# Optimization experiments

Hardware: AMD Instinct MI355X
Metric: run time of the kernel (lower is better)

Reference implementation:

```python
import jax, jax.numpy as jnp
import numpy as np

B, S, IN, H = 32, 512, 512, 1024


def setup_inputs() -> dict:
    key = jax.random.key(0)
    k1, k2, k3 = jax.random.split(key, 3)
    x = jax.random.normal(k1, (B, S, IN), dtype=jnp.float32)
    # Linear weights: [4H, fan_in], init scaled like nn.Linear (~1/sqrt(fan_in))
    W0 = jax.random.normal(k2, (4 * H, IN + H), dtype=jnp.float32) * (1.0 / np.sqrt(IN + H))
    W1 = jax.random.normal(k3, (4 * H, H + H), dtype=jnp.float32) * (1.0 / np.sqrt(H + H))
    b0 = jnp.zeros((4 * H,), dtype=jnp.float32)
    b1 = jnp.zeros((4 * H,), dtype=jnp.float32)
    return {"x": x, "W0": W0, "b0": b0, "W1": W1, "b1": b1}


def _run_layer(inp, W, b):
    """Run one unidirectional LSTM layer over time with lax.scan.

    inp: [B, S, D_in]; W: [4H, D_in+H]; b: [4H].
    Returns (outputs [B, S, H], h_n [B, H], c_n [B, H]).
    """
    h_size = W.shape[0] // 4
    bsz = inp.shape[0]

    def step(carry, x_t):
        h, c = carry
        combined = jnp.concatenate([x_t, h], axis=1)          # [B, D_in+H]
        gates = combined @ W.T + b                            # [B, 4H]
        i, f, g, o = jnp.split(gates, 4, axis=1)
        i = jax.nn.sigmoid(i)
        f = jax.nn.sigmoid(f)
        g = jnp.tanh(g)
        o = jax.nn.sigmoid(o)
        c_next = f * c + i * g
        h_next = o * jnp.tanh(c_next)
        return (h_next, c_next), h_next

    h0 = jnp.zeros((bsz, h_size), dtype=inp.dtype)
    c0 = jnp.zeros((bsz, h_size), dtype=inp.dtype)
    (h_n, c_n), ys = jax.lax.scan(step, (h0, c0), jnp.swapaxes(inp, 0, 1))
    return jnp.swapaxes(ys, 0, 1), h_n, c_n


def reference(x, W0, b0, W1, b1):
    out0, h0n, c0n = _run_layer(x, W0, b0)
    out1, h1n, c1n = _run_layer(out0, W1, b1)
    h_n = jnp.stack([h0n, h1n], axis=0)   # [num_layers, B, H]
    c_n = jnp.stack([c0n, c1n], axis=0)
    return out1[:, -1, :], h_n, c_n
```

## Files before the change

kernel.cpp:

```cpp
#include <hip/hip_runtime.h>


typedef unsigned short ushort_t;
typedef unsigned long long u64_t;
typedef __attribute__((ext_vector_type(8))) short short8;
typedef __attribute__((ext_vector_type(4))) float f32x4;
typedef __attribute__((ext_vector_type(4))) unsigned uint4v;

#define NWG       256
#define NTHREADS  512
#define SEQ       512
#define HSLOT     32768
#define FULLSLOTS 513
#define ABORT_U32 8128
#define CNT_BYTES 32768
#define POLL_MAX  6000

__device__ __forceinline__ ushort_t f2bf(float f) {
  unsigned u = __builtin_bit_cast(unsigned, f);
  u += 0x7FFFu + ((u >> 16) & 1u);
  return (ushort_t)(u >> 16);
}

__device__ __forceinline__ short8 pack_bf8(f32x4 a, f32x4 b) {
  short8 r;
  r[0] = (short)f2bf(a[0]); r[1] = (short)f2bf(a[1]);
  r[2] = (short)f2bf(a[2]); r[3] = (short)f2bf(a[3]);
  r[4] = (short)f2bf(b[0]); r[5] = (short)f2bf(b[1]);
  r[6] = (short)f2bf(b[2]); r[7] = (short)f2bf(b[3]);
  return r;
}

__device__ __forceinline__ float sigm(float x) { return 1.0f / (1.0f + __expf(-x)); }
__device__ __forceinline__ float fast_tanh(float x) {
  x = fminf(fmaxf(x, -15.f), 15.f);
  float e = __expf(-2.0f * x);
  return (1.0f - e) / (1.0f + e);
}

__device__ __forceinline__ unsigned aload(const unsigned* p) {
  return __hip_atomic_load(p, __ATOMIC_RELAXED, __HIP_MEMORY_SCOPE_AGENT);
}

template<bool COH>
__device__ __forceinline__ void load16g(f32x4* hv, const char* base) {
#pragma unroll
  for (int ch = 0; ch < 16; ++ch) {
    const char* a = base + (long)ch * 2048;
    if constexpr (COH)
      asm volatile("global_load_dwordx4 %0, %1, off sc0 sc1"
                   : "=v"(hv[ch]) : "v"(a));
    else
      asm volatile("global_load_dwordx4 %0, %1, off"
                   : "=v"(hv[ch]) : "v"(a));
  }
  asm volatile("s_waitcnt vmcnt(0)" ::: "memory");
  __builtin_amdgcn_sched_barrier(0);
}

__device__ __forceinline__ int bad16(const f32x4* hv) {
  int bad = 0;
#pragma unroll
  for (int ch = 0; ch < 16; ++ch) {
    uint4v d = __builtin_bit_cast(uint4v, hv[ch]);
    unsigned m0 = d[0] > d[1] ? d[0] : d[1];
    unsigned m1 = d[2] > d[3] ? d[2] : d[3];
    unsigned m  = m0 > m1 ? m0 : m1;
    bad |= (int)(m == 0xFFFFFFFFu);
  }
  return bad;
}

template<bool FIRSTCOH>
__device__ __forceinline__ void poll16(f32x4* hv, const char* base,
                                       unsigned* abortp) {
  load16g<FIRSTCOH>(hv, base);
  if (!__any(bad16(hv))) return;
  for (int it = 0;; ++it) {
    load16g<true>(hv, base);
    if (!__any(bad16(hv))) return;
    if ((it & 63) == 63 && aload(abortp) != 0) return;
    if (it >= POLL_MAX) {
      __hip_atomic_store(abortp, 1u, __ATOMIC_RELAXED, __HIP_MEMORY_SCOPE_AGENT);
      return;
    }
    if (it > 8) __builtin_amdgcn_s_sleep(2);
  }
}

template<int KX, bool XFP32, bool ISL1>
__device__ __forceinline__ void run_layer(
    const void* xsrc, long x_step, long x_bstride,
    const ushort_t* __restrict__ hbuf, ushort_t* __restrict__ hbuf_w,
    const float* __restrict__ W, int ldw,
    const float* __restrict__ bias,
    float* __restrict__ out, int out_h_off, int out_c_off, int write_last,
    float* xbuf, float* red, unsigned* abortp, int ub)
{
  constexpr int XCH = (KX / 2) / 32;
  const int lane  = threadIdx.x & 63;
  const int wave  = threadIdx.x >> 6;
  const int ntile = wave >> 2;
  const int r     = wave & 3;
  const bool isH  = r < 2;
  const int sub   = r & 1;
  const int wrow  = lane & 15;
  const int kg    = lane >> 4;
  const int koff  = kg * 8;
  const int bb    = ntile * 16 + (lane & 15);

  const int kbase = isH ? (KX + sub * 512) : ((r - 2) * (KX / 2));
  const int mych  = isH ? 16 : XCH;
  short8 wreg[2][16];
  #pragma unroll
  for (int mt = 0; mt < 2; ++mt) {
    const int grow = (wrow & 3) * 1024 + ub + mt * 4 + (wrow >> 2);
    const float* ws = W + (long)grow * ldw + kbase + koff;
    #pragma unroll
    for (int ch = 0; ch < 16; ++ch) {
      if (ch < mych) {
        f32x4 v0 = *(const f32x4*)(ws + ch * 32);
        f32x4 v1 = *(const f32x4*)(ws + ch * 32 + 4);
        wreg[mt][ch] = pack_bf8(v0, v1);
      }
    }
  }

  const int u0 = ub + kg;
  float bI[2], bF[2], bG[2], bO[2], c[2] = {0.f, 0.f};
  #pragma unroll
  for (int mt = 0; mt < 2; ++mt) {
    const int u = u0 + mt * 4;
    bI[mt] = bias[u];        bF[mt] = bias[1024 + u];
    bG[mt] = bias[2048 + u]; bO[mt] = bias[3072 + u];
  }

  for (int w = 0; w <= SEQ; ++w) {
    const int t = w - 1;
    f32x4 acc[2] = {{0.f,0.f,0.f,0.f},{0.f,0.f,0.f,0.f}};

    if (isH && w >= 1) {
      const char* gb = (const char*)hbuf + (long)t * (HSLOT * 2)
                     + (long)(((sub * 64 + kg) * 32 + bb) * 16);
      f32x4 hv[16];
      poll16<true>(hv, gb, abortp);
      #pragma unroll
      for (int ch = 0; ch < 16; ++ch) {
        short8 b = __builtin_bit_cast(short8, hv[ch]);
        acc[0] = __builtin_amdgcn_mfma_f32_16x16x32_bf16(wreg[0][ch], b, acc[0], 0, 0, 0);
        acc[1] = __builtin_amdgcn_mfma_f32_16x16x32_bf16(wreg[1][ch], b, acc[1], 0, 0, 0);
      }
      if (sub == 0) {
        #pragma unroll
        for (int mt = 0; mt < 2; ++mt)
          *(f32x4*)&red[((ntile * 2 + mt) * 64 + lane) * 4] = acc[mt];
      }
    }

    __syncthreads();

    if (isH && sub == 1 && w >= 1) {
      u64_t pk[2]; float hh[2];
      #pragma unroll
      for (int mt = 0; mt < 2; ++mt) {
        f32x4 a = acc[mt];
        a += *(const f32x4*)&red[((ntile * 2 + mt) * 64 + lane) * 4];
        a += *(const f32x4*)&xbuf[(((((t & 1) * 2 + ntile) * 2 + 0) * 2 + mt) * 64 + lane) * 4];
        a += *(const f32x4*)&xbuf[(((((t & 1) * 2 + ntile) * 2 + 1) * 2 + mt) * 64 + lane) * 4];
        float pi = a[0] + bI[mt], pf = a[1] + bF[mt];
        float pg = a[2] + bG[mt], po = a[3] + bO[mt];
        float ig = sigm(pi), fg = sigm(pf), gg = fast_tanh(pg), og = sigm(po);
        c[mt] = fg * c[mt] + ig * gg;
        float h = og * fast_tanh(c[mt]);
        hh[mt] = h;
        unsigned v  = f2bf(h);
        unsigned v1 = __shfl((int)v, (lane & 15) + 16);
        unsigned v2 = __shfl((int)v, (lane & 15) + 32);
        unsigned v3 = __shfl((int)v, (lane & 15) + 48);
        pk[mt] = (u64_t)(v & 0xFFFFu) | ((u64_t)(v1 & 0xFFFFu) << 16)
               | ((u64_t)(v2 & 0xFFFFu) << 32) | ((u64_t)(v3 & 0xFFFFu) << 48);
      }
      if (t == SEQ - 1) {
        #pragma unroll
        for (int mt = 0; mt < 2; ++mt) {
          const int u = u0 + mt * 4;
          out[out_h_off + bb * 1024 + u] = hh[mt];
          out[out_c_off + bb * 1024 + u] = c[mt];
          if (write_last) out[bb * 1024 + u] = hh[mt];
        }
      }
      if (lane < 16) {
        u64_t* dst = (u64_t*)((char*)hbuf_w + (long)(t + 1) * (HSLOT * 2)
                              + (long)((((ub >> 3) * 32 + bb)) * 16));
        __hip_atomic_store(dst,     pk[0], __ATOMIC_RELAXED, __HIP_MEMORY_SCOPE_AGENT);
        __hip_atomic_store(dst + 1, pk[1], __ATOMIC_RELAXED, __HIP_MEMORY_SCOPE_AGENT);
      }
    }

    if (!isH && w < SEQ) {
      const int s = w;
      f32x4 xa[2] = {{0.f,0.f,0.f,0.f},{0.f,0.f,0.f,0.f}};
      if constexpr (XFP32) {
        const float* bp = (const float*)xsrc + (long)s * x_step
                          + (long)bb * x_bstride + kbase + koff;
        f32x4 xv[2 * XCH];
        #pragma unroll
        for (int ch = 0; ch < XCH; ++ch) {
          xv[2*ch]   = *(const f32x4*)(bp + ch * 32);
          xv[2*ch+1] = *(const f32x4*)(bp + ch * 32 + 4);
        }
        #pragma unroll
        for (int ch = 0; ch < XCH; ++ch) {
          short8 bf = pack_bf8(xv[2*ch], xv[2*ch+1]);
          xa[0] = __builtin_amdgcn_mfma_f32_16x16x32_bf16(wreg[0][ch], bf, xa[0], 0, 0, 0);
          xa[1] = __builtin_amdgcn_mfma_f32_16x16x32_bf16(wreg[1][ch], bf, xa[1], 0, 0, 0);
        }
      } else {
        const char* gb = (const char*)xsrc + (long)s * (HSLOT * 2)
                       + (long)((((r - 2) * 64 + kg) * 32 + bb) * 16);
        f32x4 xv[16];
        poll16<false>(xv, gb, abortp);
        #pragma unroll
        for (int ch = 0; ch < 16; ++ch) {
          short8 b = __builtin_bit_cast(short8, xv[ch]);
          xa[0] = __builtin_amdgcn_mfma_f32_16x16x32_bf16(wreg[0][ch], b, xa[0], 0, 0, 0);
          xa[1] = __builtin_amdgcn_mfma_f32_16x16x32_bf16(wreg[1][ch], b, xa[1], 0, 0, 0);
        }
      }
      #pragma unroll
      for (int mt = 0; mt < 2; ++mt)
        *(f32x4*)&xbuf[(((((s & 1) * 2 + ntile) * 2 + (r - 2)) * 2 + mt) * 64 + lane) * 4] = xa[mt];
    }

    __syncthreads();
  }
}

__global__ __launch_bounds__(NTHREADS, 2)
void lstm_persistent(const float* __restrict__ x,  const float* __restrict__ W0,
                     const float* __restrict__ b0, const float* __restrict__ W1,
                     const float* __restrict__ b1, float* __restrict__ out,
                     unsigned* cnt, ushort_t* O0, ushort_t* H1)
{
  __shared__ float xbuf[4096];
  __shared__ float red[1024];
  const int role = (int)(blockIdx.x >> 7);
  const int ub   = (int)(blockIdx.x & 127) * 8;
  unsigned* abortp = cnt + ABORT_U32;

  if (role == 0) {
    run_layer<512, true, false>(x, 512, 262144,
                                O0, O0, W0, 1536, b0,
                                out, 32768, 98304, 0,
                                xbuf, red, abortp, ub);
  } else {
    run_layer<1024, false, true>((const void*)(O0 + HSLOT), HSLOT, 1024,
                                 H1, H1, W1, 2048, b1,
                                 out, 65536, 131072, 1,
                                 xbuf, red, abortp, ub);
  }
}

extern "C" void kernel_launch(void* const* d_in, const int* in_sizes, int n_in,
                              void* d_out, int out_size, void* d_ws, size_t ws_size,
                              hipStream_t stream) {
  (void)in_sizes; (void)n_in; (void)out_size;

  const float* x  = (const float*)d_in[0];
  const float* W0 = (const float*)d_in[1];
  const float* b0 = (const float*)d_in[2];
  const float* W1 = (const float*)d_in[3];
  const float* b1 = (const float*)d_in[4];
  float* out = (float*)d_out;

  const size_t hb_bytes = (size_t)FULLSLOTS * HSLOT * sizeof(ushort_t);
  const size_t need     = CNT_BYTES + 2 * hb_bytes;
  if (ws_size < need) return;

  unsigned* cnt = (unsigned*)d_ws;
  ushort_t* O0  = (ushort_t*)((char*)d_ws + CNT_BYTES);
  ushort_t* H1  = O0 + (size_t)FULLSLOTS * HSLOT;

  hipMemsetAsync(cnt, 0, CNT_BYTES, stream);
  hipMemsetAsync(O0, 0x00, (size_t)HSLOT * 2, stream);
  hipMemsetAsync(O0 + HSLOT, 0xFF, (size_t)(FULLSLOTS - 1) * HSLOT * 2, stream);
  hipMemsetAsync(H1, 0x00, (size_t)HSLOT * 2, stream);
  hipMemsetAsync(H1 + HSLOT, 0xFF, (size_t)(FULLSLOTS - 1) * HSLOT * 2, stream);

  lstm_persistent<<<dim3(NWG), dim3(NTHREADS), 0, stream>>>(
      x, W0, b0, W1, b1, out, cnt, O0, H1);
}
```

Measured before the change: 2.355 ms.

## Drop per-step second barrier via double-buffered reduction, split MFMA chains, prioritize recurrent waves

```diff
diff --git a/kernel.cpp b/kernel.cpp
--- a/kernel.cpp
+++ b/kernel.cpp
@@ -109,6 +109,8 @@
   const int koff  = kg * 8;
   const int bb    = ntile * 16 + (lane & 15);
 
+  if (isH) __builtin_amdgcn_s_setprio(1);
+
   const int kbase = isH ? (KX + sub * 512) : ((r - 2) * (KX / 2));
   const int mych  = isH ? 16 : XCH;
   short8 wreg[2][16];
@@ -144,16 +146,22 @@
                      + (long)(((sub * 64 + kg) * 32 + bb) * 16);
       f32x4 hv[16];
       poll16<true>(hv, gb, abortp);
+      f32x4 accB[2] = {{0.f,0.f,0.f,0.f},{0.f,0.f,0.f,0.f}};
       #pragma unroll
-      for (int ch = 0; ch < 16; ++ch) {
-        short8 b = __builtin_bit_cast(short8, hv[ch]);
-        acc[0] = __builtin_amdgcn_mfma_f32_16x16x32_bf16(wreg[0][ch], b, acc[0], 0, 0, 0);
-        acc[1] = __builtin_amdgcn_mfma_f32_16x16x32_bf16(wreg[1][ch], b, acc[1], 0, 0, 0);
-      }
+      for (int ch = 0; ch < 16; ch += 2) {
+        short8 b0 = __builtin_bit_cast(short8, hv[ch]);
+        short8 b1 = __builtin_bit_cast(short8, hv[ch + 1]);
+        acc[0]  = __builtin_amdgcn_mfma_f32_16x16x32_bf16(wreg[0][ch],   b0, acc[0], 0, 0, 0);
+        acc[1]  = __builtin_amdgcn_mfma_f32_16x16x32_bf16(wreg[1][ch],   b0, acc[1], 0, 0, 0);
+        accB[0] = __builtin_amdgcn_mfma_f32_16x16x32_bf16(wreg[0][ch+1], b1, accB[0], 0, 0, 0);
+        accB[1] = __builtin_amdgcn_mfma_f32_16x16x32_bf16(wreg[1][ch+1], b1, accB[1], 0, 0, 0);
+      }
+      acc[0] += accB[0];
+      acc[1] += accB[1];
       if (sub == 0) {
         #pragma unroll
         for (int mt = 0; mt < 2; ++mt)
-          *(f32x4*)&red[((ntile * 2 + mt) * 64 + lane) * 4] = acc[mt];
+          *(f32x4*)&red[(w & 1) * 1024 + ((ntile * 2 + mt) * 64 + lane) * 4] = acc[mt];
       }
     }
 
@@ -164,7 +172,7 @@
       #pragma unroll
       for (int mt = 0; mt < 2; ++mt) {
         f32x4 a = acc[mt];
-        a += *(const f32x4*)&red[((ntile * 2 + mt) * 64 + lane) * 4];
+        a += *(const f32x4*)&red[(w & 1) * 1024 + ((ntile * 2 + mt) * 64 + lane) * 4];
         a += *(const f32x4*)&xbuf[(((((t & 1) * 2 + ntile) * 2 + 0) * 2 + mt) * 64 + lane) * 4];
         a += *(const f32x4*)&xbuf[(((((t & 1) * 2 + ntile) * 2 + 1) * 2 + mt) * 64 + lane) * 4];
         float pi = a[0] + bI[mt], pf = a[1] + bF[mt];
@@ -199,7 +207,8 @@
 
     if (!isH && w < SEQ) {
       const int s = w;
-      f32x4 xa[2] = {{0.f,0.f,0.f,0.f},{0.f,0.f,0.f,0.f}};
+      f32x4 xa[2]  = {{0.f,0.f,0.f,0.f},{0.f,0.f,0.f,0.f}};
+      f32x4 xaB[2] = {{0.f,0.f,0.f,0.f},{0.f,0.f,0.f,0.f}};
       if constexpr (XFP32) {
         const float* bp = (const float*)xsrc + (long)s * x_step
                           + (long)bb * x_bstride + kbase + koff;
@@ -210,10 +219,13 @@
           xv[2*ch+1] = *(const f32x4*)(bp + ch * 32 + 4);
         }
         #pragma unroll
-        for (int ch = 0; ch < XCH; ++ch) {
-          short8 bf = pack_bf8(xv[2*ch], xv[2*ch+1]);
-          xa[0] = __builtin_amdgcn_mfma_f32_16x16x32_bf16(wreg[0][ch], bf, xa[0], 0, 0, 0);
-          xa[1] = __builtin_amdgcn_mfma_f32_16x16x32_bf16(wreg[1][ch], bf, xa[1], 0, 0, 0);
+        for (int ch = 0; ch < XCH; ch += 2) {
+          short8 bf0 = pack_bf8(xv[2*ch],   xv[2*ch+1]);
+          short8 bf1 = pack_bf8(xv[2*ch+2], xv[2*ch+3]);
+          xa[0]  = __builtin_amdgcn_mfma_f32_16x16x32_bf16(wreg[0][ch],   bf0, xa[0], 0, 0, 0);
+          xa[1]  = __builtin_amdgcn_mfma_f32_16x16x32_bf16(wreg[1][ch],   bf0, xa[1], 0, 0, 0);
+          xaB[0] = __builtin_amdgcn_mfma_f32_16x16x32_bf16(wreg[0][ch+1], bf1, xaB[0], 0, 0, 0);
+          xaB[1] = __builtin_amdgcn_mfma_f32_16x16x32_bf16(wreg[1][ch+1], bf1, xaB[1], 0, 0, 0);
         }
       } else {
         const char* gb = (const char*)xsrc + (long)s * (HSLOT * 2)
@@ -221,18 +233,21 @@
         f32x4 xv[16];
         poll16<false>(xv, gb, abortp);
         #pragma unroll
-        for (int ch = 0; ch < 16; ++ch) {
-          short8 b = __builtin_bit_cast(short8, xv[ch]);
-          xa[0] = __builtin_amdgcn_mfma_f32_16x16x32_bf16(wreg[0][ch], b, xa[0], 0, 0, 0);
-          xa[1] = __builtin_amdgcn_mfma_f32_16x16x32_bf16(wreg[1][ch], b, xa[1], 0, 0, 0);
+        for (int ch = 0; ch < 16; ch += 2) {
+          short8 b0 = __builtin_bit_cast(short8, xv[ch]);
+          short8 b1 = __builtin_bit_cast(short8, xv[ch + 1]);
+          xa[0]  = __builtin_amdgcn_mfma_f32_16x16x32_bf16(wreg[0][ch],   b0, xa[0], 0, 0, 0);
+          xa[1]  = __builtin_amdgcn_mfma_f32_16x16x32_bf16(wreg[1][ch],   b0, xa[1], 0, 0, 0);
+          xaB[0] = __builtin_amdgcn_mfma_f32_16x16x32_bf16(wreg[0][ch+1], b1, xaB[0], 0, 0, 0);
+          xaB[1] = __builtin_amdgcn_mfma_f32_16x16x32_bf16(wreg[1][ch+1], b1, xaB[1], 0, 0, 0);
         }
       }
+      xa[0] += xaB[0];
+      xa[1] += xaB[1];
       #pragma unroll
       for (int mt = 0; mt < 2; ++mt)
         *(f32x4*)&xbuf[(((((s & 1) * 2 + ntile) * 2 + (r - 2)) * 2 + mt) * 64 + lane) * 4] = xa[mt];
     }
-
-    __syncthreads();
   }
 }
 
@@ -243,7 +258,7 @@
                      unsigned* cnt, ushort_t* O0, ushort_t* H1)
 {
   __shared__ float xbuf[4096];
-  __shared__ float red[1024];
+  __shared__ float red[2048];
   const int role = (int)(blockIdx.x >> 7);
   const int ub   = (int)(blockIdx.x & 127) * 8;
   unsigned* abortp = cnt + ABORT_U32;
```

Result: slower. 2.831 ms (+20.2%).
